# Performance work log

Measured on AMD Instinct MI355X. Metric: run time of the kernel, lower is better.

The kernel has to match this reference:

```python
import jax, jax.numpy as jnp
import numpy as np

H = 12   # num_attention_heads
T = 8    # sample_num (frames)
D = 768  # hidden_size


def ln(x, g, b, eps=1e-12):
    m = x.mean(-1, keepdims=True)
    v = x.var(-1, keepdims=True)
    return (x - m) / jnp.sqrt(v + eps) * g + b


def attn(q, k, v):
    # q: [..., Q, Dh], k/v: [..., K, Dh]
    d = q.shape[-1]
    s = jnp.einsum('...qd,...kd->...qk', q, k) / jnp.sqrt(jnp.asarray(d, q.dtype))
    a = jax.nn.softmax(s, axis=-1)
    return jnp.einsum('...qk,...kd->...qd', a, v)


def mha_divided(x, Wq, bq, Wk, bk, Wv, bv, Wo, bo, mode):
    B, S, Dm = x.shape
    Dh = Dm // H
    P = (S - 1) // T

    def proj(W, b):
        return (x @ W + b).reshape(B, S, H, Dh).transpose(0, 2, 1, 3)  # [B,H,S,Dh]

    q, k, v = proj(Wq, bq), proj(Wk, bk), proj(Wv, bv)

    # cls token attends over the full sequence
    cls_ctx = attn(q[:, :, 0:1], k, v)                       # [B,H,1,Dh]
    cls_out = cls_ctx.transpose(0, 2, 1, 3).reshape(B, 1, Dm) @ Wo + bo

    qp = q[:, :, 1:].reshape(B, H, T, P, Dh)
    kp = k[:, :, 1:].reshape(B, H, T, P, Dh)
    vp = v[:, :, 1:].reshape(B, H, T, P, Dh)
    kc, vc = k[:, :, 0], v[:, :, 0]                          # [B,H,Dh]

    if mode == 'time':
        # each patch attends over [cls] + same patch across T frames
        qt = qp.transpose(0, 1, 3, 2, 4)                     # [B,H,P,T,Dh]
        kt = jnp.concatenate([jnp.broadcast_to(kc[:, :, None, None], (B, H, P, 1, Dh)),
                              kp.transpose(0, 1, 3, 2, 4)], axis=3)  # [B,H,P,T+1,Dh]
        vt = jnp.concatenate([jnp.broadcast_to(vc[:, :, None, None], (B, H, P, 1, Dh)),
                              vp.transpose(0, 1, 3, 2, 4)], axis=3)
        ctx = attn(qt, kt, vt)                               # [B,H,P,T,Dh]
        out = ctx.transpose(0, 3, 2, 1, 4).reshape(B, T * P, Dm)  # [B,T,P,H,Dh]
    else:  # 'space': each frame attends over [cls] + P patches in that frame
        kt = jnp.concatenate([jnp.broadcast_to(kc[:, :, None, None], (B, H, T, 1, Dh)), kp], axis=3)
        vt = jnp.concatenate([jnp.broadcast_to(vc[:, :, None, None], (B, H, T, 1, Dh)), vp], axis=3)
        ctx = attn(qp, kt, vt)                               # [B,H,T,P,Dh]
        out = ctx.transpose(0, 2, 3, 1, 4).reshape(B, T * P, Dm)
    out = out @ Wo + bo
    return jnp.concatenate([cls_out, out], axis=1)


def _forward(hidden_states,
             t_Wq, t_bq, t_Wk, t_bk, t_Wv, t_bv, t_Wo, t_bo,
             s_Wq, s_bq, s_Wk, s_bk, s_Wv, s_bv, s_Wo, s_bo,
             W1, b1, W2, b2,
             ln1_g, ln1_b, ln2_g, ln2_b, ln3_g, ln3_b):
    x = hidden_states
    # divided time attention
    x = x + mha_divided(ln(x, ln1_g, ln1_b), t_Wq, t_bq, t_Wk, t_bk, t_Wv, t_bv, t_Wo, t_bo, 'time')
    # divided space attention
    x = x + mha_divided(ln(x, ln2_g, ln2_b), s_Wq, s_bq, s_Wk, s_bk, s_Wv, s_bv, s_Wo, s_bo, 'space')
    # feed-forward with exact (erf) GELU
    h = ln(x, ln3_g, ln3_b)
    x = x + jax.nn.gelu(h @ W1 + b1, approximate=False) @ W2 + b2
    return x


def setup_inputs() -> dict:
    key = jax.random.key(0)
    ks = jax.random.split(key, 16)

    def w(k, shape, s=0.02):
        return jax.random.normal(k, shape, jnp.float32) * s

    B, S = 8, 1 + T * 196
    inp = {"hidden_states": jax.random.normal(ks[0], (B, S, D), jnp.float32)}
    names = ["t_Wq", "t_Wk", "t_Wv", "t_Wo", "s_Wq", "s_Wk", "s_Wv", "s_Wo"]
    for i, n in enumerate(names):
        inp[n] = w(ks[1 + i], (D, D))
        inp[n.replace("W", "b")] = jnp.zeros((D,), jnp.float32)
    inp["W1"] = w(ks[9], (D, 4 * D)); inp["b1"] = jnp.zeros((4 * D,), jnp.float32)
    inp["W2"] = w(ks[10], (4 * D, D)); inp["b2"] = jnp.zeros((D,), jnp.float32)
    for i in (1, 2, 3):
        inp[f"ln{i}_g"] = jnp.ones((D,), jnp.float32)
        inp[f"ln{i}_b"] = jnp.zeros((D,), jnp.float32)
    return inp


def reference(hidden_states,
              t_Wq, t_bq, t_Wk, t_bk, t_Wv, t_bv, t_Wo, t_bo,
              s_Wq, s_bq, s_Wk, s_bk, s_Wv, s_bv, s_Wo, s_bo,
              W1, b1, W2, b2,
              ln1_g, ln1_b, ln2_g, ln2_b, ln3_g, ln3_b):
    return _forward(hidden_states,
                    t_Wq, t_bq, t_Wk, t_bk, t_Wv, t_bv, t_Wo, t_bo,
                    s_Wq, s_bq, s_Wk, s_bk, s_Wv, s_bv, s_Wo, s_bo,
                    W1, b1, W2, b2,
                    ln1_g, ln1_b, ln2_g, ln2_b, ln3_g, ln3_b)
```

## Files before the change

### kernel.cpp

```cpp
#include <hip/hip_runtime.h>

#define BQ   8
#define SQ   1569
#define BS   12552
#define DM   768
#define NH   12
#define DH   64
#define TT   8
#define PP   196
#define D4   3072
#define QKVN 2304
#define CCH  24
#define CKEY 66
#define MB_PAD 104

typedef _Float16 f16;
typedef _Float16 f16x8 __attribute__((ext_vector_type(8)));
typedef float    f32x4 __attribute__((ext_vector_type(4)));
typedef unsigned long long u64;

#define AS1 __attribute__((address_space(1)))
#define AS3 __attribute__((address_space(3)))

#define Y_OFF    0ULL
#define QKV_OFF  19279872ULL
#define CTX_OFF  77119488ULL
#define H_OFF    19279872ULL
#define W_OFF    96399360ULL

__global__ __launch_bounds__(256) void ln_kernel(const float* __restrict__ x,
                                                 const float* __restrict__ g,
                                                 const float* __restrict__ bta,
                                                 f16* __restrict__ y) {
    int row = blockIdx.x * 4 + (threadIdx.x >> 6);
    int lane = threadIdx.x & 63;
    if (row >= BS) return;
    const float* xr = x + (u64)row * DM;
    float v[12];
    float s = 0.f, s2 = 0.f;
#pragma unroll
    for (int i = 0; i < 12; i++) { v[i] = xr[lane + i * 64]; s += v[i]; s2 += v[i] * v[i]; }
#pragma unroll
    for (int m = 1; m < 64; m <<= 1) { s += __shfl_xor(s, m, 64); s2 += __shfl_xor(s2, m, 64); }
    float mean = s * (1.f / 768.f);
    float var  = s2 * (1.f / 768.f) - mean * mean;
    float rstd = rsqrtf(var + 1e-12f);
    f16* yr = y + (u64)row * DM;
#pragma unroll
    for (int i = 0; i < 12; i++) {
        int c = lane + i * 64;
        yr[c] = (f16)((v[i] - mean) * rstd * g[c] + bta[c]);
    }
}

__global__ __launch_bounds__(256) void prep_kernel(const float* __restrict__ t_Wq,
                                                   const float* __restrict__ t_Wk,
                                                   const float* __restrict__ t_Wv,
                                                   const float* __restrict__ t_Wo,
                                                   const float* __restrict__ s_Wq,
                                                   const float* __restrict__ s_Wk,
                                                   const float* __restrict__ s_Wv,
                                                   const float* __restrict__ s_Wo,
                                                   const float* __restrict__ W1,
                                                   const float* __restrict__ W2,
                                                   const float* __restrict__ t_bq,
                                                   const float* __restrict__ t_bk,
                                                   const float* __restrict__ t_bv,
                                                   const float* __restrict__ s_bq,
                                                   const float* __restrict__ s_bk,
                                                   const float* __restrict__ s_bv,
                                                   f16* __restrict__ tQKV,
                                                   f16* __restrict__ tWoT,
                                                   f16* __restrict__ sQKV,
                                                   f16* __restrict__ sWoT,
                                                   f16* __restrict__ W1T,
                                                   f16* __restrict__ W2T,
                                                   float* __restrict__ tBias,
                                                   float* __restrict__ sBias) {
    int id = blockIdx.x;
    int tid = threadIdx.x;

    if (id >= 9216) {
        int j = id - 9216;
        const float* a; const float* b; const float* c; float* dst;
        if (j < 3) { a = t_bq; b = t_bk; c = t_bv; dst = tBias; }
        else       { a = s_bq; b = s_bk; c = s_bv; dst = sBias; j -= 3; }
        int i = j * 256 + tid;
        if (i < 768) { dst[i] = a[i]; dst[i + 768] = b[i]; dst[i + 1536] = c[i]; }
        return;
    }

    const float* src; f16* dst; int R, C, bx, by;
    if (id < 4608) {
        int w = id / 576, t = id % 576;
        switch (w) {
            case 0: src = t_Wq; dst = tQKV;                break;
            case 1: src = t_Wk; dst = tQKV + 768 * 768;    break;
            case 2: src = t_Wv; dst = tQKV + 2 * 768 * 768; break;
            case 3: src = t_Wo; dst = tWoT;                break;
            case 4: src = s_Wq; dst = sQKV;                break;
            case 5: src = s_Wk; dst = sQKV + 768 * 768;    break;
            case 6: src = s_Wv; dst = sQKV + 2 * 768 * 768; break;
            default: src = s_Wo; dst = sWoT;               break;
        }
        R = 768; C = 768;
        bx = (t % 24) * 32; by = (t / 24) * 32;
    } else if (id < 6912) {
        int t = id - 4608;
        src = W1; dst = W1T; R = 768; C = 3072;
        bx = (t % 96) * 32; by = (t / 96) * 32;
    } else {
        int t = id - 6912;
        src = W2; dst = W2T; R = 3072; C = 768;
        bx = (t % 24) * 32; by = (t / 24) * 32;
    }

    __shared__ float tile[32][33];
    int tx = tid & 31, ty = tid >> 5;
#pragma unroll
    for (int i = 0; i < 4; i++) {
        int r = by + ty + i * 8, c = bx + tx;
        if (r < R && c < C) tile[ty + i * 8][tx] = src[(u64)r * C + c];
    }
    __syncthreads();
#pragma unroll
    for (int i = 0; i < 4; i++) {
        int c = bx + ty + i * 8, r = by + tx;
        if (c < C && r < R) dst[(u64)c * R + r] = (f16)tile[tx][ty + i * 8];
    }
}

template <int NOUT, bool GELU, bool RESID, bool OUTF16>
__global__ __launch_bounds__(256, 4) void gemm_kernel(const f16* __restrict__ A,
                                                      const f16* __restrict__ Bt,
                                                      const float* __restrict__ bias,
                                                      const float* __restrict__ resid,
                                                      float* __restrict__ Cf,
                                                      f16* __restrict__ Ch,
                                                      int K) {
    __shared__ __align__(16) f16 As[2][128 * 32];
    __shared__ __align__(16) f16 Bs[2][128 * 32];
    int id = blockIdx.x;
    int mb = id % MB_PAD, nb = id / MB_PAD;
    if (mb >= 99) return;
    int tid  = threadIdx.x;
    int lane = tid & 63, wave = tid >> 6;
    int wm = wave >> 1, wn = wave & 1;
    int m0 = mb * 128, n0 = nb * 128;
    int l15 = lane & 15, quad = lane >> 4;

    int r0   = wave * 16 + (lane >> 2);
    int coff = (lane & 3) * 8;
    const f16* ag0 = A + (u64)(m0 + r0) * K + coff;
    const f16* ag1 = A + (u64)(m0 + r0 + 64) * K + coff;
    bool av0 = (m0 + r0) < BS, av1 = (m0 + r0 + 64) < BS;
    const f16* bg0 = Bt + (u64)(n0 + r0) * K + coff;
    const f16* bg1 = Bt + (u64)(n0 + r0 + 64) * K + coff;
    int lofs = wave * 1024;

    f32x4 acc[4][4];
#pragma unroll
    for (int i = 0; i < 4; i++)
#pragma unroll
        for (int j = 0; j < 4; j++)
#pragma unroll
            for (int r = 0; r < 4; r++) acc[i][j][r] = 0.f;

    if (av0) __builtin_amdgcn_global_load_lds((const AS1 void*)ag0, (AS3 void*)((AS3 char*)&As[0][0] + lofs), 16, 0, 0);
    if (av1) __builtin_amdgcn_global_load_lds((const AS1 void*)ag1, (AS3 void*)((AS3 char*)&As[0][0] + lofs + 4096), 16, 0, 0);
    __builtin_amdgcn_global_load_lds((const AS1 void*)bg0, (AS3 void*)((AS3 char*)&Bs[0][0] + lofs), 16, 0, 0);
    __builtin_amdgcn_global_load_lds((const AS1 void*)bg1, (AS3 void*)((AS3 char*)&Bs[0][0] + lofs + 4096), 16, 0, 0);
    ag0 += 32; ag1 += 32; bg0 += 32; bg1 += 32;

    int nit = K >> 5;
    for (int it = 0; it < nit; it++) {
        __syncthreads();
        int buf = it & 1;
        if (it + 1 < nit) {
            int nb2 = buf ^ 1;
            if (av0) __builtin_amdgcn_global_load_lds((const AS1 void*)ag0, (AS3 void*)((AS3 char*)&As[nb2][0] + lofs), 16, 0, 0);
            if (av1) __builtin_amdgcn_global_load_lds((const AS1 void*)ag1, (AS3 void*)((AS3 char*)&As[nb2][0] + lofs + 4096), 16, 0, 0);
            __builtin_amdgcn_global_load_lds((const AS1 void*)bg0, (AS3 void*)((AS3 char*)&Bs[nb2][0] + lofs), 16, 0, 0);
            __builtin_amdgcn_global_load_lds((const AS1 void*)bg1, (AS3 void*)((AS3 char*)&Bs[nb2][0] + lofs + 4096), 16, 0, 0);
            ag0 += 32; ag1 += 32; bg0 += 32; bg1 += 32;
        }
        f16x8 af[4], bf[4];
#pragma unroll
        for (int i = 0; i < 4; i++)
            af[i] = *(const f16x8*)(&As[buf][(wm * 64 + i * 16 + l15) * 32 + quad * 8]);
#pragma unroll
        for (int j = 0; j < 4; j++)
            bf[j] = *(const f16x8*)(&Bs[buf][(wn * 64 + j * 16 + l15) * 32 + quad * 8]);
#pragma unroll
        for (int i = 0; i < 4; i++)
#pragma unroll
            for (int j = 0; j < 4; j++)
                acc[i][j] = __builtin_amdgcn_mfma_f32_16x16x32_f16(af[i], bf[j], acc[i][j], 0, 0, 0);
    }

#pragma unroll
    for (int i = 0; i < 4; i++) {
#pragma unroll
        for (int j = 0; j < 4; j++) {
            int col = n0 + wn * 64 + j * 16 + l15;
            float bv = bias[col];
#pragma unroll
            for (int r = 0; r < 4; r++) {
                int row = m0 + wm * 64 + i * 16 + quad * 4 + r;
                if (row < BS) {
                    float v = acc[i][j][r] + bv;
                    if (GELU) {
                        float u = 0.7978845608028654f * (v + 0.044715f * v * v * v);
                        float e = __builtin_exp2f(-2.885390081777927f * u);
                        v = v / (1.f + e);
                    }
                    if (RESID) v += resid[(u64)row * NOUT + col];
                    if (OUTF16) Ch[(u64)row * NOUT + col] = (f16)v;
                    else        Cf[(u64)row * NOUT + col] = v;
                }
            }
        }
    }
}

__global__ __launch_bounds__(256) void attnA_kernel(const f16* __restrict__ qkv,
                                                    f16* __restrict__ ctx,
                                                    float* __restrict__ part) {
    int tid = threadIdx.x, lane = tid & 63, wave = tid >> 6;
    if (blockIdx.x < 4704) {
        int w = blockIdx.x * 4 + wave;
        int b = w / (NH * PP);
        int rem = w % (NH * PP);
        int h = rem / PP, p = rem % PP;
        u64 bb = (u64)b * SQ;
        int hoff = h * 64 + lane;

        float qv[TT], kv[9], vv[9];
#pragma unroll
        for (int t = 0; t < TT; t++) qv[t] = (float)qkv[(bb + 1 + t * PP + p) * QKVN + hoff];
        kv[0] = (float)qkv[bb * QKVN + 768 + hoff];
        vv[0] = (float)qkv[bb * QKVN + 1536 + hoff];
#pragma unroll
        for (int j = 1; j <= TT; j++) {
            u64 ro = (bb + 1 + (u64)(j - 1) * PP + p) * QKVN;
            kv[j] = (float)qkv[ro + 768 + hoff];
            vv[j] = (float)qkv[ro + 1536 + hoff];
        }
#pragma unroll
        for (int t = 0; t < TT; t++) {
            float s[9];
#pragma unroll
            for (int j = 0; j < 9; j++) {
                float ps = qv[t] * kv[j];
#pragma unroll
                for (int m = 1; m < 64; m <<= 1) ps += __shfl_xor(ps, m, 64);
                s[j] = ps * 0.125f;
            }
            float mx = s[0];
#pragma unroll
            for (int j = 1; j < 9; j++) mx = fmaxf(mx, s[j]);
            float sum = 0.f;
#pragma unroll
            for (int j = 0; j < 9; j++) { s[j] = expf(s[j] - mx); sum += s[j]; }
            float o = 0.f;
#pragma unroll
            for (int j = 0; j < 9; j++) o += s[j] * vv[j];
            o /= sum;
            ctx[(bb + 1 + (u64)t * PP + p) * DM + h * 64 + lane] = (f16)o;
        }
        return;
    }
    {
        int g = blockIdx.x - 4704;
        int c = g % CCH, bh = g / CCH;
        int b = bh / NH, h = bh % NH;
        u64 bb = (u64)b * SQ;
        __shared__ float sc[CKEY];
        __shared__ float accbuf[4][64];
        __shared__ float lbuf[4];
        __shared__ float mxs;
        float qd = (float)qkv[bb * QKVN + h * 64 + lane];
        int j0 = c * CKEY;
        int cnt = SQ - j0; if (cnt > CKEY) cnt = CKEY;
        for (int jj = wave; jj < cnt; jj += 4) {
            float p = qd * (float)qkv[(bb + j0 + jj) * QKVN + 768 + h * 64 + lane];
#pragma unroll
            for (int m = 1; m < 64; m <<= 1) p += __shfl_xor(p, m, 64);
            if (lane == 0) sc[jj] = p * 0.125f;
        }
        __syncthreads();
        if (wave == 0) {
            float m = -1e30f;
            for (int j = lane; j < cnt; j += 64) m = fmaxf(m, sc[j]);
#pragma unroll
            for (int s = 1; s < 64; s <<= 1) m = fmaxf(m, __shfl_xor(m, s, 64));
            if (lane == 0) mxs = m;
        }
        __syncthreads();
        float mx = mxs;
        float acc = 0.f, l = 0.f;
        for (int jj = wave; jj < cnt; jj += 4) {
            float w = expf(sc[jj] - mx);
            l += w;
            acc += w * (float)qkv[(bb + j0 + jj) * QKVN + 1536 + h * 64 + lane];
        }
        accbuf[wave][lane] = acc;
        if (lane == 0) lbuf[wave] = l;
        __syncthreads();
        if (tid < 64) {
            float a = accbuf[0][tid] + accbuf[1][tid] + accbuf[2][tid] + accbuf[3][tid];
            float* pb = part + ((u64)bh * CCH + c) * 66;
            if (tid == 0) { pb[0] = mxs; pb[1] = lbuf[0] + lbuf[1] + lbuf[2] + lbuf[3]; }
            pb[2 + tid] = a;
        }
    }
}

__global__ __launch_bounds__(256) void cls_part_kernel(const f16* __restrict__ qkv,
                                                       float* __restrict__ part) {
    int g = blockIdx.x;
    int c = g % CCH, bh = g / CCH;
    int b = bh / NH, h = bh % NH;
    u64 bb = (u64)b * SQ;
    int tid = threadIdx.x, lane = tid & 63, wave = tid >> 6;
    __shared__ float sc[CKEY];
    __shared__ float accbuf[4][64];
    __shared__ float lbuf[4];
    __shared__ float mxs;
    float qd = (float)qkv[bb * QKVN + h * 64 + lane];
    int j0 = c * CKEY;
    int cnt = SQ - j0; if (cnt > CKEY) cnt = CKEY;
    for (int jj = wave; jj < cnt; jj += 4) {
        float p = qd * (float)qkv[(bb + j0 + jj) * QKVN + 768 + h * 64 + lane];
#pragma unroll
        for (int m = 1; m < 64; m <<= 1) p += __shfl_xor(p, m, 64);
        if (lane == 0) sc[jj] = p * 0.125f;
    }
    __syncthreads();
    if (wave == 0) {
        float m = -1e30f;
        for (int j = lane; j < cnt; j += 64) m = fmaxf(m, sc[j]);
#pragma unroll
        for (int s = 1; s < 64; s <<= 1) m = fmaxf(m, __shfl_xor(m, s, 64));
        if (lane == 0) mxs = m;
    }
    __syncthreads();
    float mx = mxs;
    float acc = 0.f, l = 0.f;
    for (int jj = wave; jj < cnt; jj += 4) {
        float w = expf(sc[jj] - mx);
        l += w;
        acc += w * (float)qkv[(bb + j0 + jj) * QKVN + 1536 + h * 64 + lane];
    }
    accbuf[wave][lane] = acc;
    if (lane == 0) lbuf[wave] = l;
    __syncthreads();
    if (tid < 64) {
        float a = accbuf[0][tid] + accbuf[1][tid] + accbuf[2][tid] + accbuf[3][tid];
        float* pb = part + ((u64)bh * CCH + c) * 66;
        if (tid == 0) { pb[0] = mxs; pb[1] = lbuf[0] + lbuf[1] + lbuf[2] + lbuf[3]; }
        pb[2 + tid] = a;
    }
}

__global__ __launch_bounds__(256) void cls_comb_kernel(const float* __restrict__ part,
                                                       f16* __restrict__ ctx) {
    int w = blockIdx.x * 4 + (threadIdx.x >> 6);
    int lane = threadIdx.x & 63;
    if (w >= BQ * NH) return;
    int b = w / NH, h = w % NH;
    const float* pb = part + (u64)w * CCH * 66;
    float m = (lane < CCH) ? pb[lane * 66] : -1e30f;
#pragma unroll
    for (int s = 1; s < 64; s <<= 1) m = fmaxf(m, __shfl_xor(m, s, 64));
    float l = (lane < CCH) ? pb[lane * 66 + 1] * expf(pb[lane * 66] - m) : 0.f;
#pragma unroll
    for (int s = 1; s < 64; s <<= 1) l += __shfl_xor(l, s, 64);
    float o = 0.f;
    for (int j = 0; j < CCH; j++) {
        float mj = pb[j * 66];
        o += pb[j * 66 + 2 + lane] * expf(mj - m);
    }
    ctx[((u64)b * SQ) * DM + h * 64 + lane] = (f16)(o / l);
}

__global__ __launch_bounds__(256) void space_attn_kernel(const f16* __restrict__ qkv,
                                                         f16* __restrict__ ctx) {
    int g = blockIdx.x;
    int b = g / (NH * TT);
    int rem = g % (NH * TT);
    int h = rem / TT, t = rem % TT;
    __shared__ __align__(16) f16 Vt[64 * 232];
    __shared__ __align__(16) f16 Ps[4 * 16 * 232];
    u64 bb = (u64)b * SQ;
    int tid = threadIdx.x, lane = tid & 63, wave = tid >> 6;
    int l15 = lane & 15, quad = lane >> 4;

    for (int i = tid; i < 4 * 16 * 232 * 2 / 16; i += 256)
        ((uint4*)Ps)[i] = make_uint4(0u, 0u, 0u, 0u);

    for (int idx = tid; idx < 232 * 8; idx += 256) {
        int c8 = idx / 232;
        int j  = idx - c8 * 232;
        int c  = c8 * 8;
        uint4 vraw = make_uint4(0u, 0u, 0u, 0u);
        if (j < 197) {
            int tok = (j == 0) ? 0 : (1 + t * PP + (j - 1));
            vraw = *(const uint4*)(qkv + (bb + tok) * QKVN + 1536 + h * 64 + c);
        }
        f16x8 vv = *(f16x8*)&vraw;
#pragma unroll
        for (int e = 0; e < 8; e++) Vt[(c + e) * 232 + j] = vv[e];
    }
    __syncthreads();

    f16* myP = Ps + wave * 16 * 232;
    for (int qt = wave; qt < 13; qt += 4) {
        int mloc = qt * 16 + l15;
        int mc = mloc > 195 ? 195 : mloc;
        const f16* qr = qkv + (bb + 1 + (u64)t * PP + mc) * QKVN + h * 64;
        f16x8 qa0 = *(const f16x8*)(qr + quad * 8);
        f16x8 qa1 = *(const f16x8*)(qr + 32 + quad * 8);

        f32x4 s[13];
#pragma unroll
        for (int nt = 0; nt < 13; nt++) { s[nt][0] = 0.f; s[nt][1] = 0.f; s[nt][2] = 0.f; s[nt][3] = 0.f; }
#pragma unroll
        for (int nt = 0; nt < 13; nt++) {
            int n = nt * 16 + l15;
            int ncl = n > 196 ? 196 : n;
            int tok = (ncl == 0) ? 0 : (1 + t * PP + (ncl - 1));
            const f16* kr = qkv + (bb + tok) * QKVN + 768 + h * 64;
            f16x8 kb0 = *(const f16x8*)(kr + quad * 8);
            f16x8 kb1 = *(const f16x8*)(kr + 32 + quad * 8);
            s[nt] = __builtin_amdgcn_mfma_f32_16x16x32_f16(qa0, kb0, s[nt], 0, 0, 0);
            s[nt] = __builtin_amdgcn_mfma_f32_16x16x32_f16(qa1, kb1, s[nt], 0, 0, 0);
        }
        if (l15 >= 5) { s[12][0] = -1e30f; s[12][1] = -1e30f; s[12][2] = -1e30f; s[12][3] = -1e30f; }

        float mx[4] = {-1e30f, -1e30f, -1e30f, -1e30f};
#pragma unroll
        for (int nt = 0; nt < 13; nt++)
#pragma unroll
            for (int r = 0; r < 4; r++) mx[r] = fmaxf(mx[r], s[nt][r]);
#pragma unroll
        for (int m = 1; m < 16; m <<= 1)
#pragma unroll
            for (int r = 0; r < 4; r++) mx[r] = fmaxf(mx[r], __shfl_xor(mx[r], m, 64));

        float sum[4] = {0.f, 0.f, 0.f, 0.f};
#pragma unroll
        for (int nt = 0; nt < 13; nt++)
#pragma unroll
            for (int r = 0; r < 4; r++) {
                float p = exp2f((s[nt][r] - mx[r]) * 0.18033688011112042f);
                s[nt][r] = p;
                sum[r] += p;
            }
#pragma unroll
        for (int m = 1; m < 16; m <<= 1)
#pragma unroll
            for (int r = 0; r < 4; r++) sum[r] += __shfl_xor(sum[r], m, 64);

#pragma unroll
        for (int nt = 0; nt < 13; nt++)
#pragma unroll
            for (int r = 0; r < 4; r++)
                myP[(quad * 4 + r) * 232 + nt * 16 + l15] = (f16)s[nt][r];

        f32x4 o[4];
#pragma unroll
        for (int n2 = 0; n2 < 4; n2++) { o[n2][0] = 0.f; o[n2][1] = 0.f; o[n2][2] = 0.f; o[n2][3] = 0.f; }
#pragma unroll
        for (int kc = 0; kc < 7; kc++) {
            f16x8 pa = *(const f16x8*)(&myP[l15 * 232 + kc * 32 + quad * 8]);
#pragma unroll
            for (int n2 = 0; n2 < 4; n2++) {
                f16x8 vb = *(const f16x8*)(&Vt[(n2 * 16 + l15) * 232 + kc * 32 + quad * 8]);
                o[n2] = __builtin_amdgcn_mfma_f32_16x16x32_f16(pa, vb, o[n2], 0, 0, 0);
            }
        }

        float inv[4];
#pragma unroll
        for (int r = 0; r < 4; r++) inv[r] = 1.f / sum[r];
#pragma unroll
        for (int n2 = 0; n2 < 4; n2++)
#pragma unroll
            for (int r = 0; r < 4; r++) {
                int m = qt * 16 + quad * 4 + r;
                if (m < PP)
                    ctx[(bb + 1 + (u64)t * PP + m) * DM + h * 64 + n2 * 16 + l15] = (f16)(o[n2][r] * inv[r]);
            }
    }
}

extern "C" void kernel_launch(void* const* d_in, const int* in_sizes, int n_in,
                              void* d_out, int out_size, void* d_ws, size_t ws_size,
                              hipStream_t stream) {
    const float* x_in  = (const float*)d_in[0];
    const float* t_Wq  = (const float*)d_in[1];
    const float* t_bq  = (const float*)d_in[2];
    const float* t_Wk  = (const float*)d_in[3];
    const float* t_bk  = (const float*)d_in[4];
    const float* t_Wv  = (const float*)d_in[5];
    const float* t_bv  = (const float*)d_in[6];
    const float* t_Wo  = (const float*)d_in[7];
    const float* t_bo  = (const float*)d_in[8];
    const float* s_Wq  = (const float*)d_in[9];
    const float* s_bq  = (const float*)d_in[10];
    const float* s_Wk  = (const float*)d_in[11];
    const float* s_bk  = (const float*)d_in[12];
    const float* s_Wv  = (const float*)d_in[13];
    const float* s_bv  = (const float*)d_in[14];
    const float* s_Wo  = (const float*)d_in[15];
    const float* s_bo  = (const float*)d_in[16];
    const float* W1    = (const float*)d_in[17];
    const float* b1    = (const float*)d_in[18];
    const float* W2    = (const float*)d_in[19];
    const float* b2    = (const float*)d_in[20];
    const float* ln1g  = (const float*)d_in[21];
    const float* ln1b  = (const float*)d_in[22];
    const float* ln2g  = (const float*)d_in[23];
    const float* ln2b  = (const float*)d_in[24];
    const float* ln3g  = (const float*)d_in[25];
    const float* ln3b  = (const float*)d_in[26];

    char* ws = (char*)d_ws;
    f16* y    = (f16*)(ws + Y_OFF);
    f16* qkv  = (f16*)(ws + QKV_OFF);
    f16* ctx  = (f16*)(ws + CTX_OFF);
    f16* hbuf = (f16*)(ws + H_OFF);
    float* clsP = (float*)(ws + Y_OFF);
    char* wreg = ws + W_OFF;
    f16* tQKV  = (f16*)(wreg);
    f16* tWoT  = (f16*)(wreg + 3538944);
    f16* sQKV  = (f16*)(wreg + 4718592);
    f16* sWoT  = (f16*)(wreg + 8257536);
    f16* W1T   = (f16*)(wreg + 9437184);
    f16* W2T   = (f16*)(wreg + 14155776);
    float* tBias = (float*)(wreg + 18874368);
    float* sBias = (float*)(wreg + 18883584);
    float* xcur  = (float*)d_out;

    dim3 tb(256);
    prep_kernel<<<9222, tb, 0, stream>>>(t_Wq, t_Wk, t_Wv, t_Wo, s_Wq, s_Wk, s_Wv, s_Wo,
                                         W1, W2, t_bq, t_bk, t_bv, s_bq, s_bk, s_bv,
                                         tQKV, tWoT, sQKV, sWoT, W1T, W2T, tBias, sBias);

    ln_kernel<<<3138, tb, 0, stream>>>(x_in, ln1g, ln1b, y);
    gemm_kernel<QKVN, false, false, true><<<MB_PAD * 18, tb, 0, stream>>>(y, tQKV, tBias, nullptr, nullptr, qkv, 768);
    attnA_kernel<<<7008, tb, 0, stream>>>(qkv, ctx, clsP);
    cls_comb_kernel<<<24, tb, 0, stream>>>(clsP, ctx);
    gemm_kernel<DM, false, true, false><<<MB_PAD * 6, tb, 0, stream>>>(ctx, tWoT, t_bo, x_in, xcur, nullptr, 768);

    ln_kernel<<<3138, tb, 0, stream>>>(xcur, ln2g, ln2b, y);
    gemm_kernel<QKVN, false, false, true><<<MB_PAD * 18, tb, 0, stream>>>(y, sQKV, sBias, nullptr, nullptr, qkv, 768);
    space_attn_kernel<<<768, tb, 0, stream>>>(qkv, ctx);
    cls_part_kernel<<<BQ * NH * CCH, tb, 0, stream>>>(qkv, clsP);
    cls_comb_kernel<<<24, tb, 0, stream>>>(clsP, ctx);
    gemm_kernel<DM, false, true, false><<<MB_PAD * 6, tb, 0, stream>>>(ctx, sWoT, s_bo, xcur, xcur, nullptr, 768);

    ln_kernel<<<3138, tb, 0, stream>>>(xcur, ln3g, ln3b, y);
    gemm_kernel<D4, true, false, true><<<MB_PAD * 24, tb, 0, stream>>>(y, W1T, b1, nullptr, nullptr, hbuf, 768);
    gemm_kernel<DM, false, true, false><<<MB_PAD * 6, tb, 0, stream>>>(hbuf, W2T, b2, xcur, xcur, nullptr, 3072);
}
```

Before: 834.5 us.

## Fuse LayerNorms and cls-combine into neighbouring kernels via atomic last-block counters

Removes the standalone LayerNorm and cls_comb launches. LN1 now runs as extra blocks of the weight-prep kernel. LN2 and LN3 run in the output-projection GEMMs: the last N-tile block to finish each 128-row stripe, found with a global atomic counter, normalises that stripe. The cls partial-softmax combine runs in the last-arriving partial block, and the space attention and cls partial kernels are merged into one launch. This saves launch overhead and some kernel boundaries, but the LN work now sits on a serial tail inside one block per stripe and relies on threadfence/atomic ordering.

```diff
diff --git a/kernel.cpp b/kernel.cpp
--- a/kernel.cpp
+++ b/kernel.cpp
@@ -28,30 +28,7 @@
 #define H_OFF    19279872ULL
 #define W_OFF    96399360ULL
 
-__global__ __launch_bounds__(256) void ln_kernel(const float* __restrict__ x,
-                                                 const float* __restrict__ g,
-                                                 const float* __restrict__ bta,
-                                                 f16* __restrict__ y) {
-    int row = blockIdx.x * 4 + (threadIdx.x >> 6);
-    int lane = threadIdx.x & 63;
-    if (row >= BS) return;
-    const float* xr = x + (u64)row * DM;
-    float v[12];
-    float s = 0.f, s2 = 0.f;
-#pragma unroll
-    for (int i = 0; i < 12; i++) { v[i] = xr[lane + i * 64]; s += v[i]; s2 += v[i] * v[i]; }
-#pragma unroll
-    for (int m = 1; m < 64; m <<= 1) { s += __shfl_xor(s, m, 64); s2 += __shfl_xor(s2, m, 64); }
-    float mean = s * (1.f / 768.f);
-    float var  = s2 * (1.f / 768.f) - mean * mean;
-    float rstd = rsqrtf(var + 1e-12f);
-    f16* yr = y + (u64)row * DM;
-#pragma unroll
-    for (int i = 0; i < 12; i++) {
-        int c = lane + i * 64;
-        yr[c] = (f16)((v[i] - mean) * rstd * g[c] + bta[c]);
-    }
-}
+__device__ unsigned g_ctrs[512];
 
 __global__ __launch_bounds__(256) void prep_kernel(const float* __restrict__ t_Wq,
                                                    const float* __restrict__ t_Wk,
@@ -69,6 +46,10 @@
                                                    const float* __restrict__ s_bq,
                                                    const float* __restrict__ s_bk,
                                                    const float* __restrict__ s_bv,
+                                                   const float* __restrict__ x_in,
+                                                   const float* __restrict__ ln1g,
+                                                   const float* __restrict__ ln1b,
+                                                   f16* __restrict__ y,
                                                    f16* __restrict__ tQKV,
                                                    f16* __restrict__ tWoT,
                                                    f16* __restrict__ sQKV,
@@ -80,8 +61,32 @@
     int id = blockIdx.x;
     int tid = threadIdx.x;
 
+    if (id >= 9222) {
+        int row = (id - 9222) * 4 + (tid >> 6);
+        int lane = tid & 63;
+        if (row >= BS) return;
+        const float* xr = x_in + (u64)row * DM;
+        float v[12];
+        float s = 0.f, s2 = 0.f;
+#pragma unroll
+        for (int i = 0; i < 12; i++) { v[i] = xr[lane + i * 64]; s += v[i]; s2 += v[i] * v[i]; }
+#pragma unroll
+        for (int m = 1; m < 64; m <<= 1) { s += __shfl_xor(s, m, 64); s2 += __shfl_xor(s2, m, 64); }
+        float mean = s * (1.f / 768.f);
+        float var  = s2 * (1.f / 768.f) - mean * mean;
+        float rstd = rsqrtf(var + 1e-12f);
+        f16* yr = y + (u64)row * DM;
+#pragma unroll
+        for (int i = 0; i < 12; i++) {
+            int c = lane + i * 64;
+            yr[c] = (f16)((v[i] - mean) * rstd * ln1g[c] + ln1b[c]);
+        }
+        return;
+    }
+
     if (id >= 9216) {
         int j = id - 9216;
+        if (id == 9216) for (int i = tid; i < 512; i += 256) g_ctrs[i] = 0u;
         const float* a; const float* b; const float* c; float* dst;
         if (j < 3) { a = t_bq; b = t_bk; c = t_bv; dst = tBias; }
         else       { a = s_bq; b = s_bk; c = s_bv; dst = sBias; j -= 3; }
@@ -130,14 +135,18 @@
     }
 }
 
-template <int NOUT, bool GELU, bool RESID, bool OUTF16>
+template <int NOUT, bool GELU, bool RESID, bool OUTF16, bool DOLN>
 __global__ __launch_bounds__(256, 4) void gemm_kernel(const f16* __restrict__ A,
                                                       const f16* __restrict__ Bt,
                                                       const float* __restrict__ bias,
                                                       const float* __restrict__ resid,
                                                       float* __restrict__ Cf,
                                                       f16* __restrict__ Ch,
-                                                      int K) {
+                                                      int K,
+                                                      const float* __restrict__ lng,
+                                                      const float* __restrict__ lnb,
+                                                      f16* __restrict__ yout,
+                                                      int ctrBase) {
     __shared__ __align__(16) f16 As[2][128 * 32];
     __shared__ __align__(16) f16 Bs[2][128 * 32];
     int id = blockIdx.x;
@@ -221,11 +230,113 @@
             }
         }
     }
+
+    if (DOLN) {
+        __threadfence();
+        __syncthreads();
+        __shared__ unsigned sOld;
+        if (tid == 0) sOld = atomicAdd(&g_ctrs[ctrBase + mb], 1u);
+        __syncthreads();
+        if (sOld == 5u) {
+            __threadfence();
+            int lrow = m0 + (tid >> 6);
+#pragma unroll 1
+            for (int rr = 0; rr < 32; rr++, lrow += 4) {
+                if (lrow < BS) {
+                    const float* xr = Cf + (u64)lrow * DM;
+                    float v[12];
+                    float s = 0.f, s2 = 0.f;
+#pragma unroll
+                    for (int i2 = 0; i2 < 12; i2++) { v[i2] = xr[lane + i2 * 64]; s += v[i2]; s2 += v[i2] * v[i2]; }
+#pragma unroll
+                    for (int m2 = 1; m2 < 64; m2 <<= 1) { s += __shfl_xor(s, m2, 64); s2 += __shfl_xor(s2, m2, 64); }
+                    float mean = s * (1.f / 768.f);
+                    float var  = s2 * (1.f / 768.f) - mean * mean;
+                    float rstd = rsqrtf(var + 1e-12f);
+                    f16* yr = yout + (u64)lrow * DM;
+#pragma unroll
+                    for (int i2 = 0; i2 < 12; i2++) {
+                        int c2 = lane + i2 * 64;
+                        yr[c2] = (f16)((v[i2] - mean) * rstd * lng[c2] + lnb[c2]);
+                    }
+                }
+            }
+        }
+    }
+}
+
+__device__ __forceinline__ void cls_part_comb(const f16* __restrict__ qkv,
+                                              f16* __restrict__ ctx,
+                                              float* __restrict__ part,
+                                              int g, int ctrBase,
+                                              float* sc, float* accbuf, float* lbuf,
+                                              float* mxs, unsigned* cOld) {
+    int c = g % CCH, bh = g / CCH;
+    int b = bh / NH, h = bh % NH;
+    u64 bb = (u64)b * SQ;
+    int tid = threadIdx.x, lane = tid & 63, wave = tid >> 6;
+    float qd = (float)qkv[bb * QKVN + h * 64 + lane];
+    int j0 = c * CKEY;
+    int cnt = SQ - j0; if (cnt > CKEY) cnt = CKEY;
+    for (int jj = wave; jj < cnt; jj += 4) {
+        float p = qd * (float)qkv[(bb + j0 + jj) * QKVN + 768 + h * 64 + lane];
+#pragma unroll
+        for (int m = 1; m < 64; m <<= 1) p += __shfl_xor(p, m, 64);
+        if (lane == 0) sc[jj] = p * 0.125f;
+    }
+    __syncthreads();
+    if (wave == 0) {
+        float m = -1e30f;
+        for (int j = lane; j < cnt; j += 64) m = fmaxf(m, sc[j]);
+#pragma unroll
+        for (int s = 1; s < 64; s <<= 1) m = fmaxf(m, __shfl_xor(m, s, 64));
+        if (lane == 0) *mxs = m;
+    }
+    __syncthreads();
+    float mx = *mxs;
+    float acc = 0.f, l = 0.f;
+    for (int jj = wave; jj < cnt; jj += 4) {
+        float w = expf(sc[jj] - mx);
+        l += w;
+        acc += w * (float)qkv[(bb + j0 + jj) * QKVN + 1536 + h * 64 + lane];
+    }
+    accbuf[wave * 64 + lane] = acc;
+    if (lane == 0) lbuf[wave] = l;
+    __syncthreads();
+    if (tid < 64) {
+        float a = accbuf[tid] + accbuf[64 + tid] + accbuf[128 + tid] + accbuf[192 + tid];
+        float* pb = part + ((u64)bh * CCH + c) * 66;
+        if (tid == 0) { pb[0] = *mxs; pb[1] = lbuf[0] + lbuf[1] + lbuf[2] + lbuf[3]; }
+        pb[2 + tid] = a;
+    }
+    __threadfence();
+    __syncthreads();
+    if (tid == 0) *cOld = atomicAdd(&g_ctrs[ctrBase + bh], 1u);
+    __syncthreads();
+    if (*cOld == CCH - 1) {
+        __threadfence();
+        if (tid < 64) {
+            const float* pb0 = part + (u64)bh * CCH * 66;
+            float m = (lane < CCH) ? pb0[lane * 66] : -1e30f;
+#pragma unroll
+            for (int s = 1; s < 64; s <<= 1) m = fmaxf(m, __shfl_xor(m, s, 64));
+            float l2 = (lane < CCH) ? pb0[lane * 66 + 1] * expf(pb0[lane * 66] - m) : 0.f;
+#pragma unroll
+            for (int s = 1; s < 64; s <<= 1) l2 += __shfl_xor(l2, s, 64);
+            float o = 0.f;
+            for (int j = 0; j < CCH; j++) {
+                float mj = pb0[j * 66];
+                o += pb0[j * 66 + 2 + lane] * expf(mj - m);
+            }
+            ctx[((u64)b * SQ) * DM + h * 64 + lane] = (f16)(o / l2);
+        }
+    }
 }
 
 __global__ __launch_bounds__(256) void attnA_kernel(const f16* __restrict__ qkv,
                                                     f16* __restrict__ ctx,
-                                                    float* __restrict__ part) {
+                                                    float* __restrict__ part,
+                                                    int ctrBase) {
     int tid = threadIdx.x, lane = tid & 63, wave = tid >> 6;
     if (blockIdx.x < 4704) {
         int w = blockIdx.x * 4 + wave;
@@ -270,130 +381,36 @@
         }
         return;
     }
-    {
-        int g = blockIdx.x - 4704;
-        int c = g % CCH, bh = g / CCH;
-        int b = bh / NH, h = bh % NH;
-        u64 bb = (u64)b * SQ;
-        __shared__ float sc[CKEY];
-        __shared__ float accbuf[4][64];
-        __shared__ float lbuf[4];
-        __shared__ float mxs;
-        float qd = (float)qkv[bb * QKVN + h * 64 + lane];
-        int j0 = c * CKEY;
-        int cnt = SQ - j0; if (cnt > CKEY) cnt = CKEY;
-        for (int jj = wave; jj < cnt; jj += 4) {
-            float p = qd * (float)qkv[(bb + j0 + jj) * QKVN + 768 + h * 64 + lane];
-#pragma unroll
-            for (int m = 1; m < 64; m <<= 1) p += __shfl_xor(p, m, 64);
-            if (lane == 0) sc[jj] = p * 0.125f;
-        }
-        __syncthreads();
-        if (wave == 0) {
-            float m = -1e30f;
-            for (int j = lane; j < cnt; j += 64) m = fmaxf(m, sc[j]);
-#pragma unroll
-            for (int s = 1; s < 64; s <<= 1) m = fmaxf(m, __shfl_xor(m, s, 64));
-            if (lane == 0) mxs = m;
-        }
-        __syncthreads();
-        float mx = mxs;
-        float acc = 0.f, l = 0.f;
-        for (int jj = wave; jj < cnt; jj += 4) {
-            float w = expf(sc[jj] - mx);
-            l += w;
-            acc += w * (float)qkv[(bb + j0 + jj) * QKVN + 1536 + h * 64 + lane];
-        }
-        accbuf[wave][lane] = acc;
-        if (lane == 0) lbuf[wave] = l;
-        __syncthreads();
-        if (tid < 64) {
-            float a = accbuf[0][tid] + accbuf[1][tid] + accbuf[2][tid] + accbuf[3][tid];
-            float* pb = part + ((u64)bh * CCH + c) * 66;
-            if (tid == 0) { pb[0] = mxs; pb[1] = lbuf[0] + lbuf[1] + lbuf[2] + lbuf[3]; }
-            pb[2 + tid] = a;
-        }
-    }
-}
-
-__global__ __launch_bounds__(256) void cls_part_kernel(const f16* __restrict__ qkv,
-                                                       float* __restrict__ part) {
-    int g = blockIdx.x;
-    int c = g % CCH, bh = g / CCH;
-    int b = bh / NH, h = bh % NH;
-    u64 bb = (u64)b * SQ;
-    int tid = threadIdx.x, lane = tid & 63, wave = tid >> 6;
     __shared__ float sc[CKEY];
-    __shared__ float accbuf[4][64];
+    __shared__ float accbuf[4 * 64];
     __shared__ float lbuf[4];
     __shared__ float mxs;
-    float qd = (float)qkv[bb * QKVN + h * 64 + lane];
-    int j0 = c * CKEY;
-    int cnt = SQ - j0; if (cnt > CKEY) cnt = CKEY;
-    for (int jj = wave; jj < cnt; jj += 4) {
-        float p = qd * (float)qkv[(bb + j0 + jj) * QKVN + 768 + h * 64 + lane];
-#pragma unroll
-        for (int m = 1; m < 64; m <<= 1) p += __shfl_xor(p, m, 64);
-        if (lane == 0) sc[jj] = p * 0.125f;
-    }
-    __syncthreads();
-    if (wave == 0) {
-        float m = -1e30f;
-        for (int j = lane; j < cnt; j += 64) m = fmaxf(m, sc[j]);
-#pragma unroll
-        for (int s = 1; s < 64; s <<= 1) m = fmaxf(m, __shfl_xor(m, s, 64));
-        if (lane == 0) mxs = m;
-    }
-    __syncthreads();
-    float mx = mxs;
-    float acc = 0.f, l = 0.f;
-    for (int jj = wave; jj < cnt; jj += 4) {
-        float w = expf(sc[jj] - mx);
-        l += w;
-        acc += w * (float)qkv[(bb + j0 + jj) * QKVN + 1536 + h * 64 + lane];
-    }
-    accbuf[wave][lane] = acc;
-    if (lane == 0) lbuf[wave] = l;
-    __syncthreads();
-    if (tid < 64) {
-        float a = accbuf[0][tid] + accbuf[1][tid] + accbuf[2][tid] + accbuf[3][tid];
-        float* pb = part + ((u64)bh * CCH + c) * 66;
-        if (tid == 0) { pb[0] = mxs; pb[1] = lbuf[0] + lbuf[1] + lbuf[2] + lbuf[3]; }
-        pb[2 + tid] = a;
-    }
+    __shared__ unsigned cOld;
+    cls_part_comb(qkv, ctx, part, blockIdx.x - 4704, ctrBase, sc, accbuf, lbuf, &mxs, &cOld);
 }
 
-__global__ __launch_bounds__(256) void cls_comb_kernel(const float* __restrict__ part,
-                                                       f16* __restrict__ ctx) {
-    int w = blockIdx.x * 4 + (threadIdx.x >> 6);
-    int lane = threadIdx.x & 63;
-    if (w >= BQ * NH) return;
-    int b = w / NH, h = w % NH;
-    const float* pb = part + (u64)w * CCH * 66;
-    float m = (lane < CCH) ? pb[lane * 66] : -1e30f;
-#pragma unroll
-    for (int s = 1; s < 64; s <<= 1) m = fmaxf(m, __shfl_xor(m, s, 64));
-    float l = (lane < CCH) ? pb[lane * 66 + 1] * expf(pb[lane * 66] - m) : 0.f;
-#pragma unroll
-    for (int s = 1; s < 64; s <<= 1) l += __shfl_xor(l, s, 64);
-    float o = 0.f;
-    for (int j = 0; j < CCH; j++) {
-        float mj = pb[j * 66];
-        o += pb[j * 66 + 2 + lane] * expf(mj - m);
-    }
-    ctx[((u64)b * SQ) * DM + h * 64 + lane] = (f16)(o / l);
-}
-
-__global__ __launch_bounds__(256) void space_attn_kernel(const f16* __restrict__ qkv,
-                                                         f16* __restrict__ ctx) {
+__global__ __launch_bounds__(256) void attnB_kernel(const f16* __restrict__ qkv,
+                                                    f16* __restrict__ ctx,
+                                                    float* __restrict__ part,
+                                                    int ctrBase) {
+    __shared__ __align__(16) char smem[64 * 232 * 2 + 4 * 16 * 232 * 2];
+    int tid = threadIdx.x, lane = tid & 63, wave = tid >> 6;
+    if (blockIdx.x >= 768) {
+        float* sc     = (float*)smem;
+        float* accbuf = (float*)(smem + 512);
+        float* lbuf   = (float*)(smem + 1536);
+        float* mxs    = (float*)(smem + 1552);
+        unsigned* cOld = (unsigned*)(smem + 1568);
+        cls_part_comb(qkv, ctx, part, blockIdx.x - 768, ctrBase, sc, accbuf, lbuf, mxs, cOld);
+        return;
+    }
+    f16* Vt = (f16*)smem;
+    f16* Ps = (f16*)(smem + 64 * 232 * 2);
     int g = blockIdx.x;
     int b = g / (NH * TT);
     int rem = g % (NH * TT);
     int h = rem / TT, t = rem % TT;
-    __shared__ __align__(16) f16 Vt[64 * 232];
-    __shared__ __align__(16) f16 Ps[4 * 16 * 232];
     u64 bb = (u64)b * SQ;
-    int tid = threadIdx.x, lane = tid & 63, wave = tid >> 6;
     int l15 = lane & 15, quad = lane >> 4;
 
     for (int i = tid; i < 4 * 16 * 232 * 2 / 16; i += 256)
@@ -544,24 +561,16 @@
     float* xcur  = (float*)d_out;
 
     dim3 tb(256);
-    prep_kernel<<<9222, tb, 0, stream>>>(t_Wq, t_Wk, t_Wv, t_Wo, s_Wq, s_Wk, s_Wv, s_Wo,
-                                         W1, W2, t_bq, t_bk, t_bv, s_bq, s_bk, s_bv,
-                                         tQKV, tWoT, sQKV, sWoT, W1T, W2T, tBias, sBias);
-
-    ln_kernel<<<3138, tb, 0, stream>>>(x_in, ln1g, ln1b, y);
-    gemm_kernel<QKVN, false, false, true><<<MB_PAD * 18, tb, 0, stream>>>(y, tQKV, tBias, nullptr, nullptr, qkv, 768);
-    attnA_kernel<<<7008, tb, 0, stream>>>(qkv, ctx, clsP);
-    cls_comb_kernel<<<24, tb, 0, stream>>>(clsP, ctx);
-    gemm_kernel<DM, false, true, false><<<MB_PAD * 6, tb, 0, stream>>>(ctx, tWoT, t_bo, x_in, xcur, nullptr, 768);
-
-    ln_kernel<<<3138, tb, 0, stream>>>(xcur, ln2g, ln2b, y);
-    gemm_kernel<QKVN, false, false, true><<<MB_PAD * 18, tb, 0, stream>>>(y, sQKV, sBias, nullptr, nullptr, qkv, 768);
-    space_attn_kernel<<<768, tb, 0, stream>>>(qkv, ctx);
-    cls_part_kernel<<<BQ * NH * CCH, tb, 0, stream>>>(qkv, clsP);
-    cls_comb_kernel<<<24, tb, 0, stream>>>(clsP, ctx);
-    gemm_kernel<DM, false, true, false><<<MB_PAD * 6, tb, 0, stream>>>(ctx, sWoT, s_bo, xcur, xcur, nullptr, 768);
-
-    ln_kernel<<<3138, tb, 0, stream>>>(xcur, ln3g, ln3b, y);
-    gemm_kernel<D4, true, false, true><<<MB_PAD * 24, tb, 0, stream>>>(y, W1T, b1, nullptr, nullptr, hbuf, 768);
-    gemm_kernel<DM, false, true, false><<<MB_PAD * 6, tb, 0, stream>>>(hbuf, W2T, b2, xcur, xcur, nullptr, 3072);
+    prep_kernel<<<12360, tb, 0, stream>>>(t_Wq, t_Wk, t_Wv, t_Wo, s_Wq, s_Wk, s_Wv, s_Wo,
+                                          W1, W2, t_bq, t_bk, t_bv, s_bq, s_bk, s_bv,
+                                          x_in, ln1g, ln1b, y,
+                                          tQKV, tWoT, sQKV, sWoT, W1T, W2T, tBias, sBias);
+    gemm_kernel<QKVN, false, false, true, false><<<MB_PAD * 18, tb, 0, stream>>>(y, tQKV, tBias, nullptr, nullptr, qkv, 768, nullptr, nullptr, nullptr, 0);
+    attnA_kernel<<<7008, tb, 0, stream>>>(qkv, ctx, clsP, 0);
+    gemm_kernel<DM, false, true, false, true><<<MB_PAD * 6, tb, 0, stream>>>(ctx, tWoT, t_bo, x_in, xcur, nullptr, 768, ln2g, ln2b, y, 192);
+    gemm_kernel<QKVN, false, false, true, false><<<MB_PAD * 18, tb, 0, stream>>>(y, sQKV, sBias, nullptr, nullptr, qkv, 768, nullptr, nullptr, nullptr, 0);
+    attnB_kernel<<<3072, tb, 0, stream>>>(qkv, ctx, clsP, 96);
+    gemm_kernel<DM, false, true, false, true><<<MB_PAD * 6, tb, 0, stream>>>(ctx, sWoT, s_bo, xcur, xcur, nullptr, 768, ln3g, ln3b, y, 291);
+    gemm_kernel<D4, true, false, true, false><<<MB_PAD * 24, tb, 0, stream>>>(y, W1T, b1, nullptr, nullptr, hbuf, 768, nullptr, nullptr, nullptr, 0);
+    gemm_kernel<DM, false, true, false, false><<<MB_PAD * 6, tb, 0, stream>>>(hbuf, W2T, b2, xcur, xcur, nullptr, 3072, nullptr, nullptr, nullptr, 0);
 }
```

Result: slower. 1.486 ms (+78.1%).
